# Optimization experiments

Measured on AMD Instinct MI355X. Metric: run time of the kernel, lower is better.

The kernel has to match this reference:

```python
import jax, jax.numpy as jnp
import numpy as np

N_NODES = 30000
N_EDGES = 300000
N_GRAPHS = 512
SEQ = 1000
HEADS = 10
CH = 78


def setup_inputs() -> dict:
    key = jax.random.key(0)
    ks = jax.random.split(key, 20)
    def w(k, shape, scale=0.02):
        return jax.random.normal(k, shape, jnp.float32) * scale
    x = jax.random.normal(ks[0], (N_NODES, CH), jnp.float32)
    edge_index = jax.random.randint(ks[1], (2, N_EDGES), 0, N_NODES, jnp.int32)
    # every graph gets a contiguous block of nodes (sorted batch vector)
    batch = (jnp.arange(N_NODES) * N_GRAPHS // N_NODES).astype(jnp.int32)
    target = jax.random.randint(ks[2], (N_GRAPHS, SEQ), 0, 26, jnp.int32)
    return {
        "x": x, "edge_index": edge_index, "batch": batch, "target": target,
        "W_gat": w(ks[3], (CH, HEADS * CH)),
        "att_src": w(ks[4], (HEADS, CH), 0.1),
        "att_dst": w(ks[5], (HEADS, CH), 0.1),
        "b_gat": jnp.zeros((HEADS * CH,), jnp.float32),
        "W_gcn": w(ks[6], (HEADS * CH, HEADS * CH)),
        "b_gcn": jnp.zeros((HEADS * CH,), jnp.float32),
        "W_fcg1": w(ks[7], (2 * HEADS * CH, 1500)), "b_fcg1": jnp.zeros((1500,), jnp.float32),
        "W_fcg2": w(ks[8], (1500, 128)), "b_fcg2": jnp.zeros((128,), jnp.float32),
        "emb": w(ks[9], (26, 128), 1.0),
        "W_conv": w(ks[10], (32, 1000, 8)), "b_conv": jnp.zeros((32,), jnp.float32),
        "W_fcxt": w(ks[11], (32 * 121, 128)), "b_fcxt": jnp.zeros((128,), jnp.float32),
        "W_fc1": w(ks[12], (256, 1024)), "b_fc1": jnp.zeros((1024,), jnp.float32),
        "W_fc2": w(ks[13], (1024, 512)), "b_fc2": jnp.zeros((512,), jnp.float32),
        "W_out": w(ks[14], (512, 1)), "b_out": jnp.zeros((1,), jnp.float32),
    }


def reference(x, edge_index, batch, target,
              W_gat, att_src, att_dst, b_gat, W_gcn, b_gcn,
              W_fcg1, b_fcg1, W_fcg2, b_fcg2, emb, W_conv, b_conv,
              W_fcxt, b_fcxt, W_fc1, b_fc1, W_fc2, b_fc2, W_out, b_out):
    N = x.shape[0]
    loop = jnp.arange(N, dtype=edge_index.dtype)
    src = jnp.concatenate([edge_index[0], loop])  # self-loops (PyG default)
    dst = jnp.concatenate([edge_index[1], loop])

    # ---- GATConv(78 -> 78, heads=10, concat) ----
    h = (x @ W_gat).reshape(N, HEADS, CH)           # [N,H,C]
    a_s = jnp.einsum('nhc,hc->nh', h, att_src)      # [N,H]
    a_d = jnp.einsum('nhc,hc->nh', h, att_dst)
    logits = jax.nn.leaky_relu(a_s[src] + a_d[dst], 0.2)   # [E',H]
    m = jax.ops.segment_max(logits, dst, num_segments=N)
    e = jnp.exp(logits - m[dst])
    denom = jax.ops.segment_sum(e, dst, num_segments=N)
    alpha = e / (denom[dst] + 1e-16)                # per-dst softmax
    xg = jax.ops.segment_sum(h[src] * alpha[:, :, None], dst, num_segments=N)
    xg = jax.nn.relu(xg.reshape(N, HEADS * CH) + b_gat)

    # ---- GCNConv(780 -> 780), symmetric norm with self-loops ----
    deg = jax.ops.segment_sum(jnp.ones_like(dst, dtype=xg.dtype), dst, num_segments=N)
    dinv = jax.lax.rsqrt(jnp.maximum(deg, 1.0))
    norm = dinv[src] * dinv[dst]                    # [E']
    xw = xg @ W_gcn
    xg = jax.ops.segment_sum(xw[src] * norm[:, None], dst, num_segments=N) + b_gcn
    xg = jax.nn.relu(xg)

    # ---- global max + mean pooling per graph ----
    gmax = jax.ops.segment_max(xg, batch, num_segments=N_GRAPHS)
    cnt = jax.ops.segment_sum(jnp.ones((N,), xg.dtype), batch, num_segments=N_GRAPHS)
    gmean = jax.ops.segment_sum(xg, batch, num_segments=N_GRAPHS) / cnt[:, None]
    xp = jnp.concatenate([gmax, gmean], axis=1)     # [G,1560]
    xp = jax.nn.relu(xp @ W_fcg1 + b_fcg1)          # dropout = identity (eval)
    xp = xp @ W_fcg2 + b_fcg2                       # [G,128]

    # ---- protein branch ----
    xt = emb[target]                                # [G,1000,128]
    conv = jax.lax.conv_general_dilated(
        xt, W_conv, window_strides=(1,), padding='VALID',
        dimension_numbers=('NCH', 'OIH', 'NCH'))    # [G,32,121]
    conv = conv + b_conv[None, :, None]
    xt = conv.reshape(conv.shape[0], -1) @ W_fcxt + b_fcxt  # [G,128]

    # ---- joint MLP ----
    xc = jnp.concatenate([xp, xt], axis=1)          # [G,256]
    xc = jax.nn.relu(xc @ W_fc1 + b_fc1)
    xc = jax.nn.relu(xc @ W_fc2 + b_fc2)
    return xc @ W_out + b_out                       # [G,1]
```

## Files before the change

### kernel.cpp

```cpp
#include <hip/hip_runtime.h>
#include <hip/hip_bf16.h>
#include <cstdint>
#include <cstddef>

#define N_NODES 30000
#define E0      300000
#define EPRIME  330000
#define NG      512
#define SEQL    1000
#define HEADS   10
#define CHN     78
#define HC      780
#define HP      800
#define MAXD    64

typedef __attribute__((ext_vector_type(8))) short bf16x8;
typedef __attribute__((ext_vector_type(4))) float f32x4;
typedef __attribute__((ext_vector_type(8))) unsigned short u16x8;

static __device__ __forceinline__ int src_of(const int* ei, int e){
  return (e < E0) ? ei[e] : (e - E0);
}
static __device__ __forceinline__ int dst_of(const int* ei, int e){
  return (e < E0) ? ei[E0 + e] : (e - E0);
}
static __device__ __forceinline__ unsigned short f2bf(float f){
  union { float f; unsigned u; } a; a.f = f;
  unsigned r = a.u + 0x7fff + ((a.u >> 16) & 1);
  return (unsigned short)(r >> 16);
}
static __device__ __forceinline__ float bf2f(unsigned short u){
  union { unsigned u; float f; } a; a.u = ((unsigned)u) << 16; return a.f;
}
static __device__ __forceinline__ void gl_lds16(const unsigned short* g, unsigned short* l){
  __builtin_amdgcn_global_load_lds(
      (const __attribute__((address_space(1))) void*)g,
      (__attribute__((address_space(3))) void*)l,
      16, 0, 0);
}

__global__ void k_bucket(const int* __restrict__ ei, int* __restrict__ cnt, int* __restrict__ bkt){
  int e = blockIdx.x*256 + threadIdx.x;
  if (e < EPRIME){
    int d = dst_of(ei, e);
    int s = src_of(ei, e);
    int slot = atomicAdd(&cnt[d], 1);
    if (slot < MAXD) bkt[d*MAXD + slot] = s;
  }
}

static __device__ void transp_tile(const float* __restrict__ src, unsigned short* __restrict__ dst,
                                   int K, int N, int Kp, int bx, int by){
  __shared__ float t[32][33];
  int k0 = bx*32, n0 = by*32;
  int c = threadIdx.x & 31, r = threadIdx.x >> 5;
  #pragma unroll
  for (int i=0;i<4;i++){
    int k = k0 + r + i*8;
    float v = 0.f;
    if (k < K && n0 + c < N) v = src[(size_t)k*N + n0 + c];
    t[r + i*8][c] = v;
  }
  __syncthreads();
  #pragma unroll
  for (int i=0;i<4;i++){
    int nn = n0 + r + i*8;
    int kk = k0 + c;
    if (nn < N && kk < Kp) dst[(size_t)nn*Kp + kk] = f2bf(t[c][r + i*8]);
  }
}

__global__ __launch_bounds__(256) void k_prep(
    const float* __restrict__ x, unsigned short* __restrict__ xb,
    const float* __restrict__ W_gat, unsigned short* __restrict__ wgat_t,
    const float* __restrict__ W_gcn, unsigned short* __restrict__ wgcn_t,
    const float* __restrict__ W_fcg1, unsigned short* __restrict__ wfcg1_t,
    const float* __restrict__ W_conv, float* __restrict__ w2t,
    float* __restrict__ xc, float* __restrict__ t1, float* __restrict__ t2, float* __restrict__ fg1,
    const float* __restrict__ b_fcg2, const float* __restrict__ b_fcxt,
    const float* __restrict__ b_fc1, const float* __restrict__ b_fc2,
    const float* __restrict__ b_fcg1, int* __restrict__ cnt)
{
  int b = blockIdx.x;
  int tid = threadIdx.x;
  if (b < 11250){
    int idx = b*256 + tid;
    if (idx < N_NODES*96){
      int n = idx/96, k = idx - n*96;
      xb[idx] = (k < CHN) ? f2bf(x[(size_t)n*CHN + k]) : 0;
    }
    return;
  }
  b -= 11250;
  if (b < 75){ transp_tile(W_gat, wgat_t, CHN, HC, 96, b%3, b/3); return; }
  b -= 75;
  if (b < 625){ transp_tile(W_gcn, wgcn_t, HC, HC, HP, b%25, b/25); return; }
  b -= 625;
  if (b < 2303){ transp_tile(W_fcg1, wfcg1_t, 1560, 1500, 1568, b%49, b/49); return; }
  b -= 2303;
  if (b < 512){
    int g = b;
    int zi = g*256 + tid;
    if (zi < N_NODES) cnt[zi] = 0;
    if (tid < 128){
      xc[(size_t)g*256 + tid]       = b_fcg2[tid];
      xc[(size_t)g*256 + 128 + tid] = b_fcxt[tid];
    }
    for (int i = tid; i < 1024; i += 256) t1[(size_t)g*1024 + i] = b_fc1[i];
    for (int i = tid; i < 512;  i += 256) t2[(size_t)g*512  + i] = b_fc2[i];
    for (int i = tid; i < 1500; i += 256) fg1[(size_t)g*1500 + i] = b_fcg1[i];
    return;
  }
  b -= 512;
  {
    int o = tid >> 3, k = tid & 7;
    w2t[(size_t)b*256 + tid] = W_conv[(size_t)o*8000 + b*8 + k];
  }
}

__global__ __launch_bounds__(256) void k_mfma_bt(
    const unsigned short* __restrict__ A, const unsigned short* __restrict__ Bt,
    const float* __restrict__ bias, float* __restrict__ C, unsigned short* __restrict__ Cb,
    int M, int N, int Kp, int ldc, int relu,
    int ntc, int ntr, int ntk, int Kc, int accum)
{
  const int total = ntc*ntr*ntk;
  const int per = (total + 7) >> 3;
  const int b = blockIdx.x;
  const int w = (b & 7)*per + (b >> 3);
  if (w >= total) return;
  const int kt = w / (ntc*ntr);
  const int r2 = w - kt*(ntc*ntr);
  const int row_t = r2 / ntc, col_t = r2 - row_t*ntc;
  const int row0 = row_t*128, col0 = col_t*128;
  const int kbeg = kt*Kc;
  const int kend = min(kbeg + Kc, Kp);

  __shared__ unsigned short As[128*32];
  __shared__ unsigned short Bs[128*32];
  const int tid = threadIdx.x;
  const int lane = tid & 63;
  const int wv = tid >> 6;
  const int wm = wv >> 1, wn = wv & 1;
  const int quad = lane >> 4, l16 = lane & 15;
  const int srow = lane >> 2;
  const int scol = (lane & 3) * 8;

  f32x4 acc[4][4];
  #pragma unroll
  for (int mi=0;mi<4;mi++)
    #pragma unroll
    for (int ni=0;ni<4;ni++){
      acc[mi][ni][0]=0.f; acc[mi][ni][1]=0.f; acc[mi][ni][2]=0.f; acc[mi][ni][3]=0.f;
    }

  for (int k0 = kbeg; k0 < kend; k0 += 32){
    #pragma unroll
    for (int i=0;i<2;i++){
      int ch = wv*2 + i;
      int r  = ch*16 + srow;
      gl_lds16(A  + (size_t)(row0 + r)*Kp + k0 + scol, &As[ch*512]);
      gl_lds16(Bt + (size_t)(col0 + r)*Kp + k0 + scol, &Bs[ch*512]);
    }
    __syncthreads();
    bf16x8 af[4], bfr[4];
    #pragma unroll
    for (int mi=0;mi<4;mi++) af[mi]  = *(const bf16x8*)(&As[(wm*64 + mi*16 + l16)*32 + quad*8]);
    #pragma unroll
    for (int ni=0;ni<4;ni++) bfr[ni] = *(const bf16x8*)(&Bs[(wn*64 + ni*16 + l16)*32 + quad*8]);
    #pragma unroll
    for (int mi=0;mi<4;mi++)
      #pragma unroll
      for (int ni=0;ni<4;ni++)
        acc[mi][ni] = __builtin_amdgcn_mfma_f32_16x16x32_bf16(af[mi], bfr[ni], acc[mi][ni], 0,0,0);
    __syncthreads();
  }

  #pragma unroll
  for (int mi=0;mi<4;mi++){
    #pragma unroll
    for (int rr=0;rr<4;rr++){
      int row = row0 + wm*64 + mi*16 + quad*4 + rr;
      if (row >= M) continue;
      #pragma unroll
      for (int ni=0;ni<4;ni++){
        int col = col0 + wn*64 + ni*16 + l16;
        if (col >= N) continue;
        float v = acc[mi][ni][rr];
        if (accum){
          atomicAdd(&C[(size_t)row*ldc + col], v);
        } else {
          if (bias) v += bias[col];
          if (relu) v = fmaxf(v, 0.f);
          if (Cb) Cb[(size_t)row*ldc + col] = f2bf(v);
          else    C [(size_t)row*ldc + col] = v;
        }
      }
    }
  }
}

__global__ __launch_bounds__(256) void k_gemm_sk(const float* __restrict__ A, const float* __restrict__ B,
    float* __restrict__ C, int M, int N, int K, int lda, int ldb, int ldc, int Kc, int relu_a)
{
  __shared__ float As[16][34];
  __shared__ float Bs[16][64];
  const int tid = threadIdx.x;
  const int tx = tid & 15, ty = tid >> 4;
  const int row0 = blockIdx.y * 32, col0 = blockIdx.x * 64;
  const int kbeg = blockIdx.z * Kc;
  const int kend = min(kbeg + Kc, K);
  float acc[2][4];
  #pragma unroll
  for (int i=0;i<2;i++)
    #pragma unroll
    for (int j=0;j<4;j++) acc[i][j] = 0.f;

  for (int k0 = kbeg; k0 < kend; k0 += 16){
    #pragma unroll
    for (int i=0;i<2;i++){
      int idx = tid + i*256;
      int r = idx >> 4, c = idx & 15;
      int gr = row0 + r, gc = k0 + c;
      float v = (gr < M && gc < kend) ? A[(size_t)gr*lda + gc] : 0.f;
      if (relu_a) v = fmaxf(v, 0.f);
      As[c][r] = v;
    }
    #pragma unroll
    for (int i=0;i<4;i++){
      int idx = tid + i*256;
      int r = idx >> 6, c = idx & 63;
      int gr = k0 + r, gc = col0 + c;
      Bs[r][c] = (gr < kend && gc < N) ? B[(size_t)gr*ldb + gc] : 0.f;
    }
    __syncthreads();
    #pragma unroll
    for (int kk=0; kk<16; kk++){
      float a0 = As[kk][ty*2], a1 = As[kk][ty*2+1];
      float b0 = Bs[kk][tx*4], b1 = Bs[kk][tx*4+1], b2 = Bs[kk][tx*4+2], b3 = Bs[kk][tx*4+3];
      acc[0][0]+=a0*b0; acc[0][1]+=a0*b1; acc[0][2]+=a0*b2; acc[0][3]+=a0*b3;
      acc[1][0]+=a1*b0; acc[1][1]+=a1*b1; acc[1][2]+=a1*b2; acc[1][3]+=a1*b3;
    }
    __syncthreads();
  }
  #pragma unroll
  for (int i=0;i<2;i++){
    int r = row0 + ty*2 + i;
    if (r >= M) continue;
    #pragma unroll
    for (int j=0;j<4;j++){
      int c = col0 + tx*4 + j;
      if (c < N) atomicAdd(&C[(size_t)r*ldc + c], acc[i][j]);
    }
  }
}

__global__ __launch_bounds__(256) void k_attn(const unsigned short* __restrict__ hb,
    const float* __restrict__ att_src, const float* __restrict__ att_dst,
    float* __restrict__ a_s, float* __restrict__ a_d){
  __shared__ float ssrc[HC], sdst[HC];
  for (int i = threadIdx.x; i < HC; i += 256){ ssrc[i]=att_src[i]; sdst[i]=att_dst[i]; }
  __syncthreads();
  int idx = blockIdx.x*256 + threadIdx.x;
  if (idx >= N_NODES*HEADS) return;
  int hh = idx % HEADS;
  const unsigned* hp2 = (const unsigned*)(hb + (size_t)idx*CHN);
  const float* as_ = ssrc + hh*CHN;
  const float* ad_ = sdst + hh*CHN;
  float s1=0.f, s2=0.f;
  #pragma unroll 13
  for (int c2=0;c2<39;c2++){
    unsigned u = hp2[c2];
    float v0 = bf2f((unsigned short)(u & 0xffffu));
    float v1 = bf2f((unsigned short)(u >> 16));
    int c = 2*c2;
    s1 += v0*as_[c] + v1*as_[c+1];
    s2 += v0*ad_[c] + v1*ad_[c+1];
  }
  a_s[idx]=s1; a_d[idx]=s2;
}

__global__ __launch_bounds__(256) void k_gat_agg(
    const unsigned short* __restrict__ hb, const float* __restrict__ a_s, const float* __restrict__ a_d,
    const float* __restrict__ b_gat, const int* __restrict__ cnt, const int* __restrict__ bkt,
    unsigned short* __restrict__ xgb, float* __restrict__ dinv)
{
  int n = blockIdx.x;
  int deg = cnt[n];
  int degc = min(deg, MAXD);
  int tid = threadIdx.x;
  __shared__ int   s_src[MAXD];
  __shared__ float s_adn[HEADS];
  __shared__ float s_lg[MAXD*HEADS];
  __shared__ float s_al[MAXD*HEADS];
  if (tid < HEADS) s_adn[tid] = a_d[(size_t)n*HEADS + tid];
  if (tid < degc)  s_src[tid] = bkt[n*MAXD + tid];
  __syncthreads();
  for (int idx = tid; idx < degc*HEADS; idx += 256){
    int j = idx/HEADS, t = idx - j*HEADS;
    float l = a_s[(size_t)s_src[j]*HEADS + t] + s_adn[t];
    s_lg[idx] = (l > 0.f) ? l : 0.2f*l;
  }
  __syncthreads();
  if (tid < HEADS){
    float m = -3.4e38f;
    for (int j=0;j<degc;j++) m = fmaxf(m, s_lg[j*HEADS+tid]);
    float s = 0.f;
    for (int j=0;j<degc;j++){ float e = __expf(s_lg[j*HEADS+tid]-m); s_al[j*HEADS+tid]=e; s+=e; }
    float inv = 1.f/(s + 1e-16f);
    for (int j=0;j<degc;j++) s_al[j*HEADS+tid] *= inv;
  }
  __syncthreads();
  int c = tid;
  if (c < 195){
    int ch = 4*c;
    int h0 = ch/CHN, h1 = (ch+1)/CHN, h2 = (ch+2)/CHN, h3 = (ch+3)/CHN;
    float ax=0.f, ay=0.f, az=0.f, aw=0.f;
    const ushort4* h4 = (const ushort4*)hb;
    for (int j=0;j<degc;j++){
      ushort4 v = h4[(size_t)s_src[j]*195 + c];
      const float* al = &s_al[j*HEADS];
      ax += al[h0]*bf2f(v.x); ay += al[h1]*bf2f(v.y);
      az += al[h2]*bf2f(v.z); aw += al[h3]*bf2f(v.w);
    }
    ushort4 o;
    o.x = f2bf(fmaxf(ax + b_gat[ch+0], 0.f));
    o.y = f2bf(fmaxf(ay + b_gat[ch+1], 0.f));
    o.z = f2bf(fmaxf(az + b_gat[ch+2], 0.f));
    o.w = f2bf(fmaxf(aw + b_gat[ch+3], 0.f));
    *(ushort4*)(xgb + (size_t)n*HP + ch) = o;
  } else if (c < 200){
    ushort4 z = {0,0,0,0};
    *(ushort4*)(xgb + (size_t)n*HP + 4*c) = z;
  }
  if (tid == 0) dinv[n] = rsqrtf((float)deg);
}

__global__ __launch_bounds__(256) void k_gcn_agg(
    const unsigned short* __restrict__ xwb, const float* __restrict__ dinv, const float* __restrict__ b_gcn,
    const int* __restrict__ cnt, const int* __restrict__ bkt,
    unsigned short* __restrict__ xg2b)
{
  int n = blockIdx.x;
  int deg = min(cnt[n], MAXD);
  int tid = threadIdx.x;
  __shared__ int   s_src[MAXD];
  __shared__ float s_w[MAXD];
  if (tid < deg){
    int s = bkt[n*MAXD + tid];
    s_src[tid] = s;
    s_w[tid] = dinv[s];
  }
  __syncthreads();
  if (tid < 195){
    float ax=0.f, ay=0.f, az=0.f, aw=0.f;
    const ushort4* x4 = (const ushort4*)xwb;
    for (int j=0;j<deg;j++){
      ushort4 v = x4[(size_t)s_src[j]*195 + tid];
      float w = s_w[j];
      ax += w*bf2f(v.x); ay += w*bf2f(v.y); az += w*bf2f(v.z); aw += w*bf2f(v.w);
    }
    float dn = dinv[n];
    int ch = 4*tid;
    ushort4 o;
    o.x = f2bf(fmaxf(dn*ax + b_gcn[ch+0], 0.f));
    o.y = f2bf(fmaxf(dn*ay + b_gcn[ch+1], 0.f));
    o.z = f2bf(fmaxf(dn*az + b_gcn[ch+2], 0.f));
    o.w = f2bf(fmaxf(dn*aw + b_gcn[ch+3], 0.f));
    *(ushort4*)(xg2b + (size_t)n*HC + ch) = o;
  }
}

__global__ __launch_bounds__(256) void k_pool(const unsigned short* __restrict__ xg2b,
                                              unsigned short* __restrict__ xpb){
  int g = blockIdx.x;
  int n0 = (N_NODES*g + NG-1) >> 9;
  int n1 = (N_NODES*(g+1) + NG-1) >> 9;
  float inv = 1.f/(float)(n1 - n0);
  int c4 = threadIdx.x;
  if (c4 < 195){
    const ushort4* x4 = (const ushort4*)xg2b;
    float m0=-3.4e38f,m1=-3.4e38f,m2=-3.4e38f,m3=-3.4e38f;
    float s0=0.f,s1=0.f,s2=0.f,s3=0.f;
    for (int n = n0; n < n1; n++){
      ushort4 v = x4[(size_t)n*195 + c4];
      float a=bf2f(v.x), b=bf2f(v.y), c=bf2f(v.z), d=bf2f(v.w);
      m0=fmaxf(m0,a); m1=fmaxf(m1,b); m2=fmaxf(m2,c); m3=fmaxf(m3,d);
      s0+=a; s1+=b; s2+=c; s3+=d;
    }
    int ch = 4*c4;
    unsigned short* row = xpb + (size_t)g*1568;
    row[ch]=f2bf(m0); row[ch+1]=f2bf(m1); row[ch+2]=f2bf(m2); row[ch+3]=f2bf(m3);
    row[HC+ch]=f2bf(s0*inv); row[HC+ch+1]=f2bf(s1*inv);
    row[HC+ch+2]=f2bf(s2*inv); row[HC+ch+3]=f2bf(s3*inv);
  }
  if (threadIdx.x < 8) xpb[(size_t)g*1568 + 1560 + threadIdx.x] = 0;
}

__global__ __launch_bounds__(256) void k_conv(const int* __restrict__ target,
                                              const float* __restrict__ W2t,
                                              const float* __restrict__ emb, const float* __restrict__ b_conv,
                                              float* __restrict__ convf){
  int g = blockIdx.x;
  int tid = threadIdx.x;
  int o = tid >> 3;
  __shared__ int   tgt[SEQL];
  __shared__ int   cntv[26];
  __shared__ int   startv[27];
  __shared__ int   ofs[26];
  __shared__ alignas(16) unsigned short posv[SEQL];
  __shared__ float U[256*26];
  __shared__ float sE[26*128 + 32];

  for (int i = tid; i < 26*128; i += 256) sE[i] = emb[i];
  if (tid < 32) sE[26*128 + tid] = 0.f;
  if (tid < 26) cntv[tid] = 0;
  const int* tg = target + g*SEQL;
  for (int i = tid; i < SEQL; i += 256) tgt[i] = tg[i];
  __syncthreads();

  for (int i = tid; i < SEQL; i += 256) atomicAdd(&cntv[tgt[i]], 1);
  __syncthreads();
  if (tid == 0){
    int s = 0;
    #pragma unroll
    for (int v = 0; v < 26; v++){ startv[v] = s; ofs[v] = s; s += cntv[v]; }
    startv[26] = s;
  }
  __syncthreads();
  for (int i = tid; i < SEQL; i += 256){
    int v = tgt[i];
    int slot = atomicAdd(&ofs[v], 1);
    posv[slot] = (unsigned short)((v << 10) | i);
  }
  __syncthreads();

  {
    const float* wp2 = W2t + tid;
    float s = 0.f;
    int cur = 0;
    for (int j = 0; j < SEQL; j += 8){
      u16x8 p8 = *(const u16x8*)&posv[j];
      float w[8];
      #pragma unroll
      for (int q = 0; q < 8; q++) w[q] = wp2[((int)p8[q] & 1023) << 8];
      #pragma unroll
      for (int q = 0; q < 8; q++){
        int ve = (int)p8[q] >> 10;
        if (ve != cur){
          U[tid*26 + cur] = s;
          for (int z = cur+1; z < ve; z++) U[tid*26 + z] = 0.f;
          cur = ve; s = 0.f;
        }
        s += w[q];
      }
    }
    U[tid*26 + cur] = s;
    for (int z = cur+1; z < 26; z++) U[tid*26 + z] = 0.f;
  }
  __syncthreads();

  int pg = tid & 7;
  int p0 = pg * 16;
  int np = 121 - p0; if (np > 16) np = 16;
  float acc[16];
  #pragma unroll
  for (int i=0;i<16;i++) acc[i]=0.f;
  for (int v = 0; v < 26; v++){
    float u[8];
    #pragma unroll
    for (int kk=0;kk<8;kk++) u[kk] = U[(o*8 + kk)*26 + v];
    const float* ep = &sE[v*128 + p0];
    float e[24];
    #pragma unroll
    for (int i=0;i<24;i+=4){
      float4 q = *(const float4*)(ep + i);
      e[i]=q.x; e[i+1]=q.y; e[i+2]=q.z; e[i+3]=q.w;
    }
    #pragma unroll
    for (int pl=0; pl<16; pl++){
      acc[pl] += u[0]*e[pl]   + u[1]*e[pl+1] + u[2]*e[pl+2] + u[3]*e[pl+3]
               + u[4]*e[pl+4] + u[5]*e[pl+5] + u[6]*e[pl+6] + u[7]*e[pl+7];
    }
  }
  float bo = b_conv[o];
  for (int pl=0; pl<np; pl++)
    convf[(size_t)g*3872 + o*121 + p0 + pl] = acc[pl] + bo;
}

__global__ __launch_bounds__(64) void k_final(const float* __restrict__ t2, const float* __restrict__ W_out,
                                              const float* __restrict__ b_out, float* __restrict__ out){
  int g = blockIdx.x;
  int lane = threadIdx.x;
  const float* r = t2 + (size_t)g*512;
  float s = 0.f;
  #pragma unroll
  for (int i = lane; i < 512; i += 64) s += fmaxf(r[i], 0.f)*W_out[i];
  #pragma unroll
  for (int off=32; off; off>>=1) s += __shfl_down(s, off);
  if (lane==0) out[g] = s + b_out[0];
}

extern "C" void kernel_launch(void* const* d_in, const int* in_sizes, int n_in,
                              void* d_out, int out_size, void* d_ws, size_t ws_size,
                              hipStream_t stream) {
  const float* x      = (const float*)d_in[0];
  const int*   ei     = (const int*)  d_in[1];
  const int*   target = (const int*)  d_in[3];
  const float* W_gat  = (const float*)d_in[4];
  const float* att_src= (const float*)d_in[5];
  const float* att_dst= (const float*)d_in[6];
  const float* b_gat  = (const float*)d_in[7];
  const float* W_gcn  = (const float*)d_in[8];
  const float* b_gcn  = (const float*)d_in[9];
  const float* W_fcg1 = (const float*)d_in[10];
  const float* b_fcg1 = (const float*)d_in[11];
  const float* W_fcg2 = (const float*)d_in[12];
  const float* b_fcg2 = (const float*)d_in[13];
  const float* emb    = (const float*)d_in[14];
  const float* W_conv = (const float*)d_in[15];
  const float* b_conv = (const float*)d_in[16];
  const float* W_fcxt = (const float*)d_in[17];
  const float* b_fcxt = (const float*)d_in[18];
  const float* W_fc1  = (const float*)d_in[19];
  const float* b_fc1  = (const float*)d_in[20];
  const float* W_fc2  = (const float*)d_in[21];
  const float* b_fc2  = (const float*)d_in[22];
  const float* W_out  = (const float*)d_in[23];
  const float* b_out  = (const float*)d_in[24];
  float* out = (float*)d_out;

  char* ws = (char*)d_ws;
  size_t off = 0;
  auto alloc = [&](size_t bytes)->char*{
    char* p = ws + off;
    off += (bytes + 255) & ~(size_t)255;
    return p;
  };
  unsigned short* hb  = (unsigned short*)alloc((size_t)N_NODES*HC*2);
  unsigned short* xwb = (unsigned short*)alloc((size_t)N_NODES*HC*2);
  unsigned short* xu  = (unsigned short*)alloc((size_t)N_NODES*HP*2);
  unsigned short* xb     = (unsigned short*)alloc((size_t)N_NODES*96*2);
  unsigned short* wgat_t = (unsigned short*)alloc((size_t)HC*96*2);
  unsigned short* wgcn_t = (unsigned short*)alloc((size_t)HC*HP*2);
  unsigned short* wfcg1_t= (unsigned short*)alloc((size_t)1500*1568*2);
  unsigned short* xpb    = (unsigned short*)alloc((size_t)NG*1568*2);
  float* a_s    = (float*)alloc((size_t)N_NODES*HEADS*4);
  float* a_d    = (float*)alloc((size_t)N_NODES*HEADS*4);
  float* dinv   = (float*)alloc((size_t)N_NODES*4);
  int*   cnt    = (int*)  alloc((size_t)N_NODES*4);
  int*   bkt    = (int*)  alloc((size_t)N_NODES*MAXD*4);
  float* fg1    = (float*)alloc((size_t)NG*1500*4);
  float* convf  = (float*)alloc((size_t)NG*3872*4);
  float* xc     = (float*)alloc((size_t)NG*256*4);
  float* t1     = (float*)alloc((size_t)NG*1024*4);
  float* t2     = (float*)alloc((size_t)NG*512*4);
  float* w2t    = (float*)alloc((size_t)SEQL*256*4);

  unsigned short* xgb  = xu;
  unsigned short* xg2b = xu;

  k_prep<<<11250+75+625+2303+512+1000, 256, 0, stream>>>(
      x, xb, W_gat, wgat_t, W_gcn, wgcn_t, W_fcg1, wfcg1_t, W_conv, w2t,
      xc, t1, t2, fg1, b_fcg2, b_fcxt, b_fc1, b_fc2, b_fcg1, cnt);

  k_bucket<<<(EPRIME+255)/256, 256, 0, stream>>>(ei, cnt, bkt);

  auto swgrid = [](int total){ return 8 * ((total + 7) / 8); };

  k_mfma_bt<<<swgrid(7*235), 256, 0, stream>>>(xb, wgat_t, nullptr, nullptr, hb,
                                               N_NODES, HC, 96, HC, 0, 7, 235, 1, 96, 0);
  k_attn<<<(N_NODES*HEADS+255)/256, 256, 0, stream>>>(hb, att_src, att_dst, a_s, a_d);
  k_gat_agg<<<N_NODES, 256, 0, stream>>>(hb, a_s, a_d, b_gat, cnt, bkt, xgb, dinv);

  k_mfma_bt<<<swgrid(7*235), 256, 0, stream>>>(xgb, wgcn_t, nullptr, nullptr, xwb,
                                               N_NODES, HC, HP, HC, 0, 7, 235, 1, HP, 0);
  k_gcn_agg<<<N_NODES, 256, 0, stream>>>(xwb, dinv, b_gcn, cnt, bkt, xg2b);

  k_pool<<<NG, 256, 0, stream>>>(xg2b, xpb);
  k_mfma_bt<<<swgrid(12*4*2), 256, 0, stream>>>(xpb, wfcg1_t, nullptr, fg1, nullptr,
                                                NG, 1500, 1568, 1500, 0, 12, 4, 2, 800, 1);
  k_gemm_sk<<<dim3(2, 16, 8), 256, 0, stream>>>(fg1, W_fcg2, xc, NG, 128, 1500, 1500, 128, 256, 192, 1);

  k_conv<<<NG, 256, 0, stream>>>(target, w2t, emb, b_conv, convf);
  k_gemm_sk<<<dim3(2, 16, 8), 256, 0, stream>>>(convf, W_fcxt, xc + 128, NG, 128, 3872, 3872, 128, 256, 512, 0);

  k_gemm_sk<<<dim3(16, 16, 1), 256, 0, stream>>>(xc, W_fc1, t1, NG, 1024, 256, 256, 1024, 1024, 256, 0);
  k_gemm_sk<<<dim3(8, 16, 2), 256, 0, stream>>>(t1, W_fc2, t2, NG, 512, 1024, 1024, 512, 512, 512, 1);
  k_final<<<NG, 64, 0, stream>>>(t2, W_out, b_out, out);
}
```

Before: 826.3 us.

## Pad node feature rows to 800 and process two nodes per aggregation block

The hb and xwb intermediates now use a padded row stride of 800, and their pad columns are zeroed in the prep kernel. This lets the GAT and GCN aggregation kernels gather 16-byte vectors (8 bf16) per thread instead of 8-byte vectors. Each 256-thread block now handles two nodes with 128 threads each, halving the grid and using the threads better, since only 98 lanes per node do work. It adds extra memory for the padding and per-element head selection logic in the GAT gather.

```diff
diff --git a/kernel.cpp b/kernel.cpp
--- a/kernel.cpp
+++ b/kernel.cpp
@@ -76,6 +76,7 @@
     const float* __restrict__ W_gcn, unsigned short* __restrict__ wgcn_t,
     const float* __restrict__ W_fcg1, unsigned short* __restrict__ wfcg1_t,
     const float* __restrict__ W_conv, float* __restrict__ w2t,
+    unsigned short* __restrict__ hbp, unsigned short* __restrict__ xwbp,
     float* __restrict__ xc, float* __restrict__ t1, float* __restrict__ t2, float* __restrict__ fg1,
     const float* __restrict__ b_fcg2, const float* __restrict__ b_fcxt,
     const float* __restrict__ b_fc1, const float* __restrict__ b_fc2,
@@ -109,6 +110,13 @@
     for (int i = tid; i < 1024; i += 256) t1[(size_t)g*1024 + i] = b_fc1[i];
     for (int i = tid; i < 512;  i += 256) t2[(size_t)g*512  + i] = b_fc2[i];
     for (int i = tid; i < 1500; i += 256) fg1[(size_t)g*1500 + i] = b_fcg1[i];
+    for (int i = tid; i < 59; i += 256){
+      int n = g + i*512;
+      if (n < N_NODES){
+        *reinterpret_cast<unsigned long long*>(hbp  + (size_t)n*HP + HC) = 0ull;
+        *reinterpret_cast<unsigned long long*>(xwbp + (size_t)n*HP + HC) = 0ull;
+      }
+    }
     return;
   }
   b -= 512;
@@ -263,8 +271,9 @@
   __syncthreads();
   int idx = blockIdx.x*256 + threadIdx.x;
   if (idx >= N_NODES*HEADS) return;
-  int hh = idx % HEADS;
-  const unsigned* hp2 = (const unsigned*)(hb + (size_t)idx*CHN);
+  int n  = idx / HEADS;
+  int hh = idx - n*HEADS;
+  const unsigned* hp2 = (const unsigned*)(hb + (size_t)n*HP + hh*CHN);
   const float* as_ = ssrc + hh*CHN;
   const float* ad_ = sdst + hh*CHN;
   float s1=0.f, s2=0.f;
@@ -285,55 +294,75 @@
     const float* __restrict__ b_gat, const int* __restrict__ cnt, const int* __restrict__ bkt,
     unsigned short* __restrict__ xgb, float* __restrict__ dinv)
 {
-  int n = blockIdx.x;
+  int half = threadIdx.x >> 7;
+  int lt   = threadIdx.x & 127;
+  int n = blockIdx.x*2 + half;
   int deg = cnt[n];
   int degc = min(deg, MAXD);
-  int tid = threadIdx.x;
-  __shared__ int   s_src[MAXD];
-  __shared__ float s_adn[HEADS];
-  __shared__ float s_lg[MAXD*HEADS];
-  __shared__ float s_al[MAXD*HEADS];
-  if (tid < HEADS) s_adn[tid] = a_d[(size_t)n*HEADS + tid];
-  if (tid < degc)  s_src[tid] = bkt[n*MAXD + tid];
-  __syncthreads();
-  for (int idx = tid; idx < degc*HEADS; idx += 256){
+  __shared__ int   s_src[2][MAXD];
+  __shared__ float s_adn[2][HEADS];
+  __shared__ float s_lg[2][MAXD*HEADS];
+  __shared__ float s_al[2][MAXD*HEADS];
+  if (lt < HEADS) s_adn[half][lt] = a_d[(size_t)n*HEADS + lt];
+  if (lt < degc)  s_src[half][lt] = bkt[n*MAXD + lt];
+  __syncthreads();
+  for (int idx = lt; idx < degc*HEADS; idx += 128){
     int j = idx/HEADS, t = idx - j*HEADS;
-    float l = a_s[(size_t)s_src[j]*HEADS + t] + s_adn[t];
-    s_lg[idx] = (l > 0.f) ? l : 0.2f*l;
-  }
-  __syncthreads();
-  if (tid < HEADS){
+    float l = a_s[(size_t)s_src[half][j]*HEADS + t] + s_adn[half][t];
+    s_lg[half][idx] = (l > 0.f) ? l : 0.2f*l;
+  }
+  __syncthreads();
+  if (lt < HEADS){
     float m = -3.4e38f;
-    for (int j=0;j<degc;j++) m = fmaxf(m, s_lg[j*HEADS+tid]);
+    for (int j=0;j<degc;j++) m = fmaxf(m, s_lg[half][j*HEADS+lt]);
     float s = 0.f;
-    for (int j=0;j<degc;j++){ float e = __expf(s_lg[j*HEADS+tid]-m); s_al[j*HEADS+tid]=e; s+=e; }
+    for (int j=0;j<degc;j++){ float e = __expf(s_lg[half][j*HEADS+lt]-m); s_al[half][j*HEADS+lt]=e; s+=e; }
     float inv = 1.f/(s + 1e-16f);
-    for (int j=0;j<degc;j++) s_al[j*HEADS+tid] *= inv;
-  }
-  __syncthreads();
-  int c = tid;
-  if (c < 195){
-    int ch = 4*c;
-    int h0 = ch/CHN, h1 = (ch+1)/CHN, h2 = (ch+2)/CHN, h3 = (ch+3)/CHN;
-    float ax=0.f, ay=0.f, az=0.f, aw=0.f;
-    const ushort4* h4 = (const ushort4*)hb;
-    for (int j=0;j<degc;j++){
-      ushort4 v = h4[(size_t)s_src[j]*195 + c];
-      const float* al = &s_al[j*HEADS];
-      ax += al[h0]*bf2f(v.x); ay += al[h1]*bf2f(v.y);
-      az += al[h2]*bf2f(v.z); aw += al[h3]*bf2f(v.w);
-    }
-    ushort4 o;
-    o.x = f2bf(fmaxf(ax + b_gat[ch+0], 0.f));
-    o.y = f2bf(fmaxf(ay + b_gat[ch+1], 0.f));
-    o.z = f2bf(fmaxf(az + b_gat[ch+2], 0.f));
-    o.w = f2bf(fmaxf(aw + b_gat[ch+3], 0.f));
-    *(ushort4*)(xgb + (size_t)n*HP + ch) = o;
-  } else if (c < 200){
-    ushort4 z = {0,0,0,0};
-    *(ushort4*)(xgb + (size_t)n*HP + 4*c) = z;
-  }
-  if (tid == 0) dinv[n] = rsqrtf((float)deg);
+    for (int j=0;j<degc;j++) s_al[half][j*HEADS+lt] *= inv;
+  }
+  __syncthreads();
+  if (lt < 98){
+    int ch0 = lt*8;
+    int hlo = min(ch0/CHN, HEADS-1);
+    int hhi = min((ch0+7)/CHN, HEADS-1);
+    int m   = hhi*CHN - ch0;
+    const float* al = &s_al[half][0];
+    float acc[8];
+    #pragma unroll
+    for (int e=0;e<8;e++) acc[e]=0.f;
+    auto edge = [&](int j){
+      int s = s_src[half][j];
+      uint4 v = *((const uint4*)(hb + (size_t)s*HP) + lt);
+      float alo = al[j*HEADS + hlo];
+      float ahi = al[j*HEADS + hhi];
+      unsigned uu[4] = {v.x, v.y, v.z, v.w};
+      #pragma unroll
+      for (int e2=0;e2<4;e2++){
+        float v0 = bf2f((unsigned short)(uu[e2] & 0xffffu));
+        float v1 = bf2f((unsigned short)(uu[e2] >> 16));
+        float a0 = (2*e2   < m) ? alo : ahi;
+        float a1 = (2*e2+1 < m) ? alo : ahi;
+        acc[2*e2]   += a0*v0;
+        acc[2*e2+1] += a1*v1;
+      }
+    };
+    int j = 0;
+    for (; j+2 <= degc; j += 2){ edge(j); edge(j+1); }
+    for (; j < degc; ++j) edge(j);
+    u16x8 o;
+    #pragma unroll
+    for (int e=0;e<8;e++){
+      int ch = ch0+e;
+      float bv = (ch < HC) ? b_gat[ch] : 0.f;
+      float ov = (ch < HC) ? fmaxf(acc[e]+bv, 0.f) : 0.f;
+      o[e] = f2bf(ov);
+    }
+    *((u16x8*)(xgb + (size_t)n*HP) + lt) = o;
+  } else if (lt < 100){
+    u16x8 z = {0,0,0,0,0,0,0,0};
+    *((u16x8*)(xgb + (size_t)n*HP) + lt) = z;
+  }
+  if (lt == 0) dinv[n] = rsqrtf((float)deg);
 }
 
 __global__ __launch_bounds__(256) void k_gcn_agg(
@@ -341,33 +370,52 @@
     const int* __restrict__ cnt, const int* __restrict__ bkt,
     unsigned short* __restrict__ xg2b)
 {
-  int n = blockIdx.x;
+  int half = threadIdx.x >> 7;
+  int lt   = threadIdx.x & 127;
+  int n = blockIdx.x*2 + half;
   int deg = min(cnt[n], MAXD);
-  int tid = threadIdx.x;
-  __shared__ int   s_src[MAXD];
-  __shared__ float s_w[MAXD];
-  if (tid < deg){
-    int s = bkt[n*MAXD + tid];
-    s_src[tid] = s;
-    s_w[tid] = dinv[s];
-  }
-  __syncthreads();
-  if (tid < 195){
-    float ax=0.f, ay=0.f, az=0.f, aw=0.f;
-    const ushort4* x4 = (const ushort4*)xwb;
-    for (int j=0;j<deg;j++){
-      ushort4 v = x4[(size_t)s_src[j]*195 + tid];
-      float w = s_w[j];
-      ax += w*bf2f(v.x); ay += w*bf2f(v.y); az += w*bf2f(v.z); aw += w*bf2f(v.w);
-    }
+  __shared__ int   s_src[2][MAXD];
+  __shared__ float s_w[2][MAXD];
+  if (lt < deg){
+    int s = bkt[n*MAXD + lt];
+    s_src[half][lt] = s;
+    s_w[half][lt] = dinv[s];
+  }
+  __syncthreads();
+  if (lt < 98){
+    int ch0 = lt*8;
+    float acc[8];
+    #pragma unroll
+    for (int e=0;e<8;e++) acc[e]=0.f;
+    auto edge = [&](int j){
+      int s = s_src[half][j];
+      float w = s_w[half][j];
+      uint4 v = *((const uint4*)(xwb + (size_t)s*HP) + lt);
+      unsigned uu[4] = {v.x, v.y, v.z, v.w};
+      #pragma unroll
+      for (int e2=0;e2<4;e2++){
+        acc[2*e2]   += w*bf2f((unsigned short)(uu[e2] & 0xffffu));
+        acc[2*e2+1] += w*bf2f((unsigned short)(uu[e2] >> 16));
+      }
+    };
+    int j = 0;
+    for (; j+2 <= deg; j += 2){ edge(j); edge(j+1); }
+    for (; j < deg; ++j) edge(j);
     float dn = dinv[n];
-    int ch = 4*tid;
-    ushort4 o;
-    o.x = f2bf(fmaxf(dn*ax + b_gcn[ch+0], 0.f));
-    o.y = f2bf(fmaxf(dn*ay + b_gcn[ch+1], 0.f));
-    o.z = f2bf(fmaxf(dn*az + b_gcn[ch+2], 0.f));
-    o.w = f2bf(fmaxf(dn*aw + b_gcn[ch+3], 0.f));
-    *(ushort4*)(xg2b + (size_t)n*HC + ch) = o;
+    ushort4 o0, o1;
+    float r0 = fmaxf(dn*acc[0] + ((ch0   < HC) ? b_gcn[ch0  ] : 0.f), 0.f);
+    float r1 = fmaxf(dn*acc[1] + ((ch0+1 < HC) ? b_gcn[ch0+1] : 0.f), 0.f);
+    float r2 = fmaxf(dn*acc[2] + ((ch0+2 < HC) ? b_gcn[ch0+2] : 0.f), 0.f);
+    float r3 = fmaxf(dn*acc[3] + ((ch0+3 < HC) ? b_gcn[ch0+3] : 0.f), 0.f);
+    float r4 = fmaxf(dn*acc[4] + ((ch0+4 < HC) ? b_gcn[ch0+4] : 0.f), 0.f);
+    float r5 = fmaxf(dn*acc[5] + ((ch0+5 < HC) ? b_gcn[ch0+5] : 0.f), 0.f);
+    float r6 = fmaxf(dn*acc[6] + ((ch0+6 < HC) ? b_gcn[ch0+6] : 0.f), 0.f);
+    float r7 = fmaxf(dn*acc[7] + ((ch0+7 < HC) ? b_gcn[ch0+7] : 0.f), 0.f);
+    o0.x=f2bf(r0); o0.y=f2bf(r1); o0.z=f2bf(r2); o0.w=f2bf(r3);
+    o1.x=f2bf(r4); o1.y=f2bf(r5); o1.z=f2bf(r6); o1.w=f2bf(r7);
+    unsigned short* row = xg2b + (size_t)n*HC;
+    *(ushort4*)(row + ch0) = o0;
+    if (ch0+4 < HC) *(ushort4*)(row + ch0+4) = o1;
   }
 }
 
@@ -537,8 +585,8 @@
     off += (bytes + 255) & ~(size_t)255;
     return p;
   };
-  unsigned short* hb  = (unsigned short*)alloc((size_t)N_NODES*HC*2);
-  unsigned short* xwb = (unsigned short*)alloc((size_t)N_NODES*HC*2);
+  unsigned short* hb  = (unsigned short*)alloc((size_t)N_NODES*HP*2);
+  unsigned short* xwb = (unsigned short*)alloc((size_t)N_NODES*HP*2);
   unsigned short* xu  = (unsigned short*)alloc((size_t)N_NODES*HP*2);
   unsigned short* xb     = (unsigned short*)alloc((size_t)N_NODES*96*2);
   unsigned short* wgat_t = (unsigned short*)alloc((size_t)HC*96*2);
@@ -561,7 +609,7 @@
   unsigned short* xg2b = xu;
 
   k_prep<<<11250+75+625+2303+512+1000, 256, 0, stream>>>(
-      x, xb, W_gat, wgat_t, W_gcn, wgcn_t, W_fcg1, wfcg1_t, W_conv, w2t,
+      x, xb, W_gat, wgat_t, W_gcn, wgcn_t, W_fcg1, wfcg1_t, W_conv, w2t, hb, xwb,
       xc, t1, t2, fg1, b_fcg2, b_fcxt, b_fc1, b_fc2, b_fcg1, cnt);
 
   k_bucket<<<(EPRIME+255)/256, 256, 0, stream>>>(ei, cnt, bkt);
@@ -569,13 +617,13 @@
   auto swgrid = [](int total){ return 8 * ((total + 7) / 8); };
 
   k_mfma_bt<<<swgrid(7*235), 256, 0, stream>>>(xb, wgat_t, nullptr, nullptr, hb,
-                                               N_NODES, HC, 96, HC, 0, 7, 235, 1, 96, 0);
+                                               N_NODES, HC, 96, HP, 0, 7, 235, 1, 96, 0);
   k_attn<<<(N_NODES*HEADS+255)/256, 256, 0, stream>>>(hb, att_src, att_dst, a_s, a_d);
-  k_gat_agg<<<N_NODES, 256, 0, stream>>>(hb, a_s, a_d, b_gat, cnt, bkt, xgb, dinv);
+  k_gat_agg<<<N_NODES/2, 256, 0, stream>>>(hb, a_s, a_d, b_gat, cnt, bkt, xgb, dinv);
 
   k_mfma_bt<<<swgrid(7*235), 256, 0, stream>>>(xgb, wgcn_t, nullptr, nullptr, xwb,
-                                               N_NODES, HC, HP, HC, 0, 7, 235, 1, HP, 0);
-  k_gcn_agg<<<N_NODES, 256, 0, stream>>>(xwb, dinv, b_gcn, cnt, bkt, xg2b);
+                                               N_NODES, HC, HP, HP, 0, 7, 235, 1, HP, 0);
+  k_gcn_agg<<<N_NODES/2, 256, 0, stream>>>(xwb, dinv, b_gcn, cnt, bkt, xg2b);
 
   k_pool<<<NG, 256, 0, stream>>>(xg2b, xpb);
   k_mfma_bt<<<swgrid(12*4*2), 256, 0, stream>>>(xpb, wfcg1_t, nullptr, fg1, nullptr,
```

Result: no change. 824.3 us (-0.2%).
